# Optimization experiments

Measured on AMD Instinct MI355X. Metric: run time of the kernel, lower is better.

The kernel has to match this reference:

```python
import jax, jax.numpy as jnp
import numpy as np

B, S, D = 4, 2048, 1024
H, HD = 16, 64
MLP = 4 * D
EPS = 1e-6


def _rms_norm(x, scale):
    var = jnp.mean(jnp.square(x), axis=-1, keepdims=True)
    return x * jax.lax.rsqrt(var + EPS) * scale


def setup_inputs() -> dict:
    key = jax.random.key(0)
    ks = jax.random.split(key, 8)
    sd = D ** -0.5
    return {
        "x": jax.random.normal(ks[0], (B, S, D), jnp.float32),
        "pre_norm_scale": jnp.ones((D,), jnp.float32),
        "w_mlp_in": jax.random.normal(ks[1], (D, MLP), jnp.float32) * sd,   # MLPBlockInput, no bias
        "wq": jax.random.normal(ks[2], (D, H, HD), jnp.float32) * sd,
        "wk": jax.random.normal(ks[3], (D, H, HD), jnp.float32) * sd,
        "wv": jax.random.normal(ks[4], (D, H, HD), jnp.float32) * sd,
        "w_mlp_out": jax.random.normal(ks[5], (MLP, D), jnp.float32) * (MLP ** -0.5),
        "b_mlp_out": jnp.zeros((D,), jnp.float32),
        "w_attn_out": jax.random.normal(ks[6], (H, HD, D), jnp.float32) * sd,  # DenseGeneral axis=(-2,-1)
        "b_attn_out": jnp.zeros((D,), jnp.float32),
    }


def reference(x, pre_norm_scale, w_mlp_in, wq, wk, wv, w_mlp_out, b_mlp_out,
              w_attn_out, b_attn_out):
    residual = x
    xn = _rms_norm(x, pre_norm_scale)                      # pre_norm (TPNorm)

    # QKVMLPDense: fused MLP-input + QKV projections
    h = jax.nn.gelu(jnp.einsum("bsd,df->bsf", xn, w_mlp_in))   # [B,S,MLP]
    q = jnp.einsum("bsd,dhk->bshk", xn, wq)                    # [B,S,H,HD]
    k = jnp.einsum("bsd,dhk->bshk", xn, wk)
    v = jnp.einsum("bsd,dhk->bshk", xn, wv)

    # dot_product_attention (mask=None)
    scores = jnp.einsum("bqhd,bkhd->bhqk", q, k) / jnp.sqrt(jnp.asarray(HD, x.dtype))
    probs = jax.nn.softmax(scores, axis=-1)
    attn_v = jnp.einsum("bhqk,bkhd->bqhd", probs, v)           # [B,S,H,HD]

    # AttnMLPOut: mlp_out + attn_out
    mlp_out = jnp.einsum("bsf,fd->bsd", h, w_mlp_out) + b_mlp_out
    attn_out = jnp.einsum("bqhk,hkd->bqd", attn_v, w_attn_out) + b_attn_out
    block_out = mlp_out + attn_out                              # dropout is identity (train=False)
    return residual + block_out
```

## Files before the change

### kernel.cpp

```cpp
#include <hip/hip_runtime.h>
#include <cstdint>
#include <cstddef>

typedef float floatx4 __attribute__((ext_vector_type(4)));
typedef short bf16x8 __attribute__((ext_vector_type(8)));

#define MFMA(a, b, c) __builtin_amdgcn_mfma_f32_16x16x32_bf16((a), (b), (c), 0, 0, 0)

__device__ __forceinline__ unsigned short f2bf(float f) {
  union { float f; unsigned int u; } v; v.f = f;
  unsigned int u = v.u;
  unsigned int r = (u + 0x7FFFu + ((u >> 16) & 1u)) >> 16;
  return (unsigned short)r;
}

__device__ __forceinline__ void gload_lds16(const unsigned short* g, unsigned short* s) {
  __builtin_amdgcn_global_load_lds(
      (const __attribute__((address_space(1))) unsigned int*)g,
      (__attribute__((address_space(3))) unsigned int*)s, 16, 0, 0);
}

__global__ __launch_bounds__(256) void transpose_all(
    const float* __restrict__ w_mlp_in, const float* __restrict__ wq,
    const float* __restrict__ wk, const float* __restrict__ wv,
    const float* __restrict__ w_mlp_out, const float* __restrict__ w_attn_out,
    unsigned short* __restrict__ wcatT, unsigned short* __restrict__ wcat2T) {
  int id = blockIdx.x;
  const float* src; unsigned short* dst; int C, ldd, bx, by, q;
  if (id < 4096)       { src = w_mlp_in;   dst = wcatT;                        C = 4096; ldd = 1024; q = id;         bx = q & 127; by = q >> 7; }
  else if (id < 5120)  { src = wq;         dst = wcatT + (size_t)4096 * 1024;  C = 1024; ldd = 1024; q = id - 4096;  bx = q & 31;  by = q >> 5; }
  else if (id < 6144)  { src = wk;         dst = wcatT + (size_t)5120 * 1024;  C = 1024; ldd = 1024; q = id - 5120;  bx = q & 31;  by = q >> 5; }
  else if (id < 7168)  { src = wv;         dst = wcatT + (size_t)6144 * 1024;  C = 1024; ldd = 1024; q = id - 6144;  bx = q & 31;  by = q >> 5; }
  else if (id < 11264) { src = w_mlp_out;  dst = wcat2T;                       C = 1024; ldd = 5120; q = id - 7168;  bx = q & 31;  by = q >> 5; }
  else                 { src = w_attn_out; dst = wcat2T + 4096;                C = 1024; ldd = 5120; q = id - 11264; bx = q & 31;  by = q >> 5; }
  __shared__ float tile[32][33];
  int tx = threadIdx.x & 31, ty = threadIdx.x >> 5;
#pragma unroll
  for (int i = 0; i < 4; i++) {
    int r = ty + i * 8;
    tile[r][tx] = src[(size_t)(by * 32 + r) * C + bx * 32 + tx];
  }
  __syncthreads();
#pragma unroll
  for (int i = 0; i < 4; i++) {
    int r = ty + i * 8;
    dst[(size_t)(bx * 32 + r) * ldd + by * 32 + tx] = f2bf(tile[tx][r]);
  }
}

__global__ __launch_bounds__(256) void rmsnorm_kernel(
    const float* __restrict__ x, const float* __restrict__ scale,
    unsigned short* __restrict__ xn) {
  int row = blockIdx.x;
  const float4 v = ((const float4*)(x + (size_t)row * 1024))[threadIdx.x];
  float ss = v.x * v.x + v.y * v.y + v.z * v.z + v.w * v.w;
#pragma unroll
  for (int off = 1; off < 64; off <<= 1) ss += __shfl_xor(ss, off, 64);
  __shared__ float ws4[4];
  if ((threadIdx.x & 63) == 0) ws4[threadIdx.x >> 6] = ss;
  __syncthreads();
  float tot = ws4[0] + ws4[1] + ws4[2] + ws4[3];
  float rs = rsqrtf(tot * (1.0f / 1024.0f) + 1e-6f);
  const float4 sc = ((const float4*)scale)[threadIdx.x];
  uint2 o;
  o.x = (unsigned)f2bf(v.x * rs * sc.x) | ((unsigned)f2bf(v.y * rs * sc.y) << 16);
  o.y = (unsigned)f2bf(v.z * rs * sc.z) | ((unsigned)f2bf(v.w * rs * sc.w) << 16);
  ((uint2*)(xn + (size_t)row * 1024))[threadIdx.x] = o;
}

template <int MODE>
__global__ __launch_bounds__(256, 2) void gemm_bt(
    const unsigned short* __restrict__ A, const unsigned short* __restrict__ BT,
    int K, void* __restrict__ outp,
    const float* __restrict__ bias1, const float* __restrict__ bias2,
    const float* __restrict__ resid,
    int msplit, int tm, int tn,
    unsigned short* __restrict__ q_out, unsigned short* __restrict__ k_out,
    unsigned short* __restrict__ v_out) {
  __shared__ unsigned short As[2][128 * 32];
  __shared__ unsigned short Bs[2][128 * 32];

  int id = blockIdx.x + gridDim.x * blockIdx.y;
  int xcd = id & 7, j = id >> 3;
  int mh = xcd % msplit, nq = xcd / msplit;
  int by = mh * tm + j / tn;
  int bx = nq * tn + j % tn;
  int m0 = by * 128, n0 = bx * 128;

  int t = threadIdx.x, lane = t & 63, wave = t >> 6;
  int l15 = lane & 15, quad = lane >> 4;
  int wm = (wave & 1) * 64, wn = (wave >> 1) * 64;

  floatx4 acc[4][4] = {};

  int lr = lane >> 2;
  int lg = (lane & 3) ^ ((lane >> 3) & 3);
  int ch0 = wave * 2, ch1 = wave * 2 + 1;
  const unsigned short* gA0 = A + (size_t)(m0 + ch0 * 16 + lr) * K + lg * 8;
  const unsigned short* gA1 = A + (size_t)(m0 + ch1 * 16 + lr) * K + lg * 8;
  const unsigned short* gB0 = BT + (size_t)(n0 + ch0 * 16 + lr) * K + lg * 8;
  const unsigned short* gB1 = BT + (size_t)(n0 + ch1 * 16 + lr) * K + lg * 8;
  unsigned short* sA0[2] = {&As[0][ch0 * 512 + lane * 8], &As[1][ch0 * 512 + lane * 8]};
  unsigned short* sA1[2] = {&As[0][ch1 * 512 + lane * 8], &As[1][ch1 * 512 + lane * 8]};
  unsigned short* sB0[2] = {&Bs[0][ch0 * 512 + lane * 8], &Bs[1][ch0 * 512 + lane * 8]};
  unsigned short* sB1[2] = {&Bs[0][ch1 * 512 + lane * 8], &Bs[1][ch1 * 512 + lane * 8]};

  int fo = (4 * l15 + (quad ^ ((l15 >> 1) & 3))) * 8;
  int ca = (wm >> 4);
  int cb = (wn >> 4);

  for (int kt = 0; kt < K; kt += 64) {
    __syncthreads();
#pragma unroll
    for (int kk = 0; kk < 2; kk++) {
      int kg = kt + kk * 32;
      gload_lds16(gA0 + kg, sA0[kk]);
      gload_lds16(gA1 + kg, sA1[kk]);
      gload_lds16(gB0 + kg, sB0[kk]);
      gload_lds16(gB1 + kg, sB1[kk]);
    }
    __syncthreads();
#pragma unroll
    for (int kk = 0; kk < 2; kk++) {
      bf16x8 a[4], b[4];
#pragma unroll
      for (int im = 0; im < 4; im++)
        a[im] = *(const bf16x8*)&As[kk][(ca + im) * 512 + fo];
#pragma unroll
      for (int in_ = 0; in_ < 4; in_++)
        b[in_] = *(const bf16x8*)&Bs[kk][(cb + in_) * 512 + fo];
#pragma unroll
      for (int im = 0; im < 4; im++)
#pragma unroll
        for (int in_ = 0; in_ < 4; in_++)
          acc[im][in_] = MFMA(a[im], b[in_], acc[im][in_]);
    }
  }

#pragma unroll
  for (int im = 0; im < 4; im++) {
#pragma unroll
    for (int in_ = 0; in_ < 4; in_++) {
#pragma unroll
      for (int r = 0; r < 4; r++) {
        int row = m0 + wm + im * 16 + quad * 4 + r;
        int col = n0 + wn + in_ * 16 + l15;
        float v = acc[im][in_][r];
        if constexpr (MODE == 6) {
          if (n0 < 4096) {
            float z = 0.7978845608028654f * (v + 0.044715f * v * v * v);
            float e = __expf(2.0f * z);
            float th = 1.0f - 2.0f / (e + 1.0f);
            ((unsigned short*)outp)[(size_t)row * 5120 + col] = f2bf(0.5f * v * (1.0f + th));
          } else {
            int seg = (n0 - 4096) >> 10;
            int cs = col - 4096 - (seg << 10);
            int b_ = row >> 11, s = row & 2047, h = cs >> 6, hd = cs & 63;
            if (seg == 0)
              q_out[(((size_t)(b_ * 16 + h)) * 2048 + s) * 64 + hd] = f2bf(v * 0.125f);
            else if (seg == 1)
              k_out[(((size_t)(b_ * 16 + h)) * 2048 + s) * 64 + hd] = f2bf(v);
            else
              v_out[(((size_t)(b_ * 16 + h)) * 64 + hd) * 2048 + s] = f2bf(v);
          }
        } else {
          size_t idx = (size_t)row * 1024 + col;
          ((float*)outp)[idx] = v + bias1[col] + bias2[col] + resid[idx];
        }
      }
    }
  }
}

__global__ __launch_bounds__(256, 2) void flash_attn(
    const unsigned short* __restrict__ q_buf, const unsigned short* __restrict__ k_buf,
    const unsigned short* __restrict__ v_buf, unsigned short* __restrict__ cat) {
  constexpr int S = 2048, HD = 64;
  constexpr int LK = 72, LV = 72, LP = 68;
  __shared__ unsigned short Ks[64 * LK];
  __shared__ unsigned short Vs[64 * LV];
  __shared__ unsigned short Ps[4][32 * LP];

  int id = blockIdx.x + gridDim.x * blockIdx.y;
  int xcd = id & 7, j = id >> 3;
  int bh = xcd * 8 + (j >> 4);
  int qbk = j & 15;

  int t = threadIdx.x, lane = t & 63, wave = t >> 6;
  int l15 = lane & 15, quad = lane >> 4;

  const unsigned short* qp = q_buf + (size_t)bh * S * HD;
  const unsigned short* kp = k_buf + (size_t)bh * S * HD;
  const unsigned short* vp = v_buf + (size_t)bh * HD * S;

  int q0 = qbk * 128 + wave * 32;
  bf16x8 aQ[2][2];
#pragma unroll
  for (int qf = 0; qf < 2; qf++) {
    aQ[qf][0] = *(const bf16x8*)&qp[(size_t)(q0 + qf * 16 + l15) * HD + quad * 8];
    aQ[qf][1] = *(const bf16x8*)&qp[(size_t)(q0 + qf * 16 + l15) * HD + 32 + quad * 8];
  }

  floatx4 acc_o[2][4] = {};
  float lrow[2][4] = {};

  int kr = t >> 3, kc = (t & 7) * 8;

  uint4 rK0 = *(const uint4*)&kp[(size_t)kr * HD + kc];
  uint4 rK1 = *(const uint4*)&kp[(size_t)(kr + 32) * HD + kc];
  uint4 rV0 = *(const uint4*)&vp[(size_t)kr * S + kc];
  uint4 rV1 = *(const uint4*)&vp[(size_t)(kr + 32) * S + kc];

  for (int kv = 0; kv < S; kv += 64) {
    __syncthreads();
    *(uint4*)&Ks[kr * LK + kc] = rK0;
    *(uint4*)&Ks[(kr + 32) * LK + kc] = rK1;
    *(uint4*)&Vs[kr * LV + kc] = rV0;
    *(uint4*)&Vs[(kr + 32) * LV + kc] = rV1;
    __syncthreads();
    if (kv + 64 < S) {
      rK0 = *(const uint4*)&kp[(size_t)(kv + 64 + kr) * HD + kc];
      rK1 = *(const uint4*)&kp[(size_t)(kv + 64 + kr + 32) * HD + kc];
      rV0 = *(const uint4*)&vp[(size_t)kr * S + kv + 64 + kc];
      rV1 = *(const uint4*)&vp[(size_t)(kr + 32) * S + kv + 64 + kc];
    }

    floatx4 z[2][4];
#pragma unroll
    for (int cg = 0; cg < 4; cg++) {
      bf16x8 bk0 = *(const bf16x8*)&Ks[(cg * 16 + l15) * LK + quad * 8];
      bf16x8 bk1 = *(const bf16x8*)&Ks[(cg * 16 + l15) * LK + 32 + quad * 8];
#pragma unroll
      for (int qf = 0; qf < 2; qf++) {
        floatx4 acc = {};
        acc = MFMA(aQ[qf][0], bk0, acc);
        acc = MFMA(aQ[qf][1], bk1, acc);
        z[qf][cg] = acc;
      }
    }
#pragma unroll
    for (int qf = 0; qf < 2; qf++)
#pragma unroll
      for (int cg = 0; cg < 4; cg++)
#pragma unroll
        for (int r = 0; r < 4; r++) {
          float e = __expf(z[qf][cg][r]);
          lrow[qf][r] += e;
          Ps[wave][(qf * 16 + quad * 4 + r) * LP + cg * 16 + l15] = f2bf(e);
        }
    asm volatile("s_waitcnt lgkmcnt(0)" ::: "memory");
#pragma unroll
    for (int c = 0; c < 2; c++) {
      bf16x8 aP[2];
#pragma unroll
      for (int qf = 0; qf < 2; qf++) {
        const unsigned short* pp = &Ps[wave][(qf * 16 + l15) * LP + c * 32 + quad * 8];
        ((uint2*)&aP[qf])[0] = *(const uint2*)pp;
        ((uint2*)&aP[qf])[1] = *(const uint2*)(pp + 4);
      }
#pragma unroll
      for (int n = 0; n < 4; n++) {
        bf16x8 bv = *(const bf16x8*)&Vs[(n * 16 + l15) * LV + c * 32 + quad * 8];
        acc_o[0][n] = MFMA(aP[0], bv, acc_o[0][n]);
        acc_o[1][n] = MFMA(aP[1], bv, acc_o[1][n]);
      }
    }
  }

#pragma unroll
  for (int qf = 0; qf < 2; qf++)
#pragma unroll
    for (int r = 0; r < 4; r++) {
      float s = lrow[qf][r];
#pragma unroll
      for (int off = 1; off < 16; off <<= 1) s += __shfl_xor(s, off, 16);
      lrow[qf][r] = s;
    }

  int b_ = bh >> 4, h = bh & 15;
#pragma unroll
  for (int qf = 0; qf < 2; qf++)
#pragma unroll
    for (int r = 0; r < 4; r++) {
      float inv = 1.0f / lrow[qf][r];
      int srow = q0 + qf * 16 + quad * 4 + r;
      size_t base = ((size_t)(b_ * 2048 + srow)) * 5120 + 4096 + h * 64;
#pragma unroll
      for (int n = 0; n < 4; n++)
        cat[base + n * 16 + l15] = f2bf(acc_o[qf][n][r] * inv);
    }
}

extern "C" void kernel_launch(void* const* d_in, const int* in_sizes, int n_in,
                              void* d_out, int out_size, void* d_ws, size_t ws_size,
                              hipStream_t stream) {
  (void)in_sizes; (void)n_in; (void)out_size; (void)ws_size;
  const float* x          = (const float*)d_in[0];
  const float* pns        = (const float*)d_in[1];
  const float* w_mlp_in   = (const float*)d_in[2];
  const float* wq         = (const float*)d_in[3];
  const float* wk         = (const float*)d_in[4];
  const float* wv         = (const float*)d_in[5];
  const float* w_mlp_out  = (const float*)d_in[6];
  const float* b_mlp_out  = (const float*)d_in[7];
  const float* w_attn_out = (const float*)d_in[8];
  const float* b_attn_out = (const float*)d_in[9];
  float* out = (float*)d_out;

  char* ws = (char*)d_ws;
  size_t off = 0;
  auto alloc = [&](size_t bytes) {
    void* p = ws + off;
    off += (bytes + 255) & ~(size_t)255;
    return p;
  };
  const size_t M = 8192;
  unsigned short* xn     = (unsigned short*)alloc(M * 1024 * 2);
  unsigned short* wcatT  = (unsigned short*)alloc((size_t)7168 * 1024 * 2);
  unsigned short* wcat2T = (unsigned short*)alloc((size_t)1024 * 5120 * 2);
  unsigned short* cat    = (unsigned short*)alloc(M * 5120 * 2);
  unsigned short* qb     = (unsigned short*)alloc(M * 1024 * 2);
  unsigned short* kb     = (unsigned short*)alloc(M * 1024 * 2);
  unsigned short* vb     = (unsigned short*)alloc(M * 1024 * 2);

  transpose_all<<<dim3(12288), 256, 0, stream>>>(
      w_mlp_in, wq, wk, wv, w_mlp_out, w_attn_out, wcatT, wcat2T);

  rmsnorm_kernel<<<dim3(8192), 256, 0, stream>>>(x, pns, xn);

  gemm_bt<6><<<dim3(56, 64), 256, 0, stream>>>(
      xn, wcatT, 1024, cat, nullptr, nullptr, nullptr, 2, 32, 14, qb, kb, vb);

  flash_attn<<<dim3(16, 64), 256, 0, stream>>>(qb, kb, vb, cat);

  gemm_bt<7><<<dim3(8, 64), 256, 0, stream>>>(
      cat, wcat2T, 5120, out, b_mlp_out, b_attn_out, x, 2, 32, 2, nullptr, nullptr, nullptr);
}
```

Before: 537.9 us.

## Use 256x256 tile GEMM with 8 waves and interleaved async LDS prefetch

Both dense GEMMs move from 128x128 tiles with 4 waves to 256x256 tiles with 8 waves. The main loop is split into four MFMA phases, and global-to-LDS loads for the next k-steps are issued between phases, guarded by explicit barriers, waitcnt and s_setprio. The goal is more operand reuse per LDS byte and better overlap of memory with compute. The trade-off is far fewer blocks: the second GEMM gets only 128 blocks across 256 CUs, which risks poor occupancy and tail effects.

Result: slower. 601.1 us (+11.8%).

```diff
diff --git a/kernel.cpp b/kernel.cpp
--- a/kernel.cpp
+++ b/kernel.cpp
@@ -6,6 +6,8 @@
 typedef short bf16x8 __attribute__((ext_vector_type(8)));
 
 #define MFMA(a, b, c) __builtin_amdgcn_mfma_f32_16x16x32_bf16((a), (b), (c), 0, 0, 0)
+#define BARRIER() __builtin_amdgcn_s_barrier()
+#define LGKM0() asm volatile("s_waitcnt lgkmcnt(0)" ::: "memory")
 
 __device__ __forceinline__ unsigned short f2bf(float f) {
   union { float f; unsigned int u; } v; v.f = f;
@@ -69,7 +71,7 @@
 }
 
 template <int MODE>
-__global__ __launch_bounds__(256, 2) void gemm_bt(
+__global__ __launch_bounds__(512, 2) void gemm256_bt(
     const unsigned short* __restrict__ A, const unsigned short* __restrict__ BT,
     int K, void* __restrict__ outp,
     const float* __restrict__ bias1, const float* __restrict__ bias2,
@@ -77,74 +79,136 @@
     int msplit, int tm, int tn,
     unsigned short* __restrict__ q_out, unsigned short* __restrict__ k_out,
     unsigned short* __restrict__ v_out) {
-  __shared__ unsigned short As[2][128 * 32];
-  __shared__ unsigned short Bs[2][128 * 32];
+  __shared__ unsigned short As[2][2][16][512];
+  __shared__ unsigned short Bs[2][2][16][512];
 
   int id = blockIdx.x + gridDim.x * blockIdx.y;
   int xcd = id & 7, j = id >> 3;
   int mh = xcd % msplit, nq = xcd / msplit;
   int by = mh * tm + j / tn;
   int bx = nq * tn + j % tn;
-  int m0 = by * 128, n0 = bx * 128;
-
-  int t = threadIdx.x, lane = t & 63, wave = t >> 6;
+  int m0 = by * 256, n0 = bx * 256;
+
+  int tid = threadIdx.x, lane = tid & 63, wave = tid >> 6;
   int l15 = lane & 15, quad = lane >> 4;
-  int wm = (wave & 1) * 64, wn = (wave >> 1) * 64;
-
-  floatx4 acc[4][4] = {};
+  int wm = wave >> 2, wn = wave & 3;
 
   int lr = lane >> 2;
   int lg = (lane & 3) ^ ((lane >> 3) & 3);
-  int ch0 = wave * 2, ch1 = wave * 2 + 1;
-  const unsigned short* gA0 = A + (size_t)(m0 + ch0 * 16 + lr) * K + lg * 8;
-  const unsigned short* gA1 = A + (size_t)(m0 + ch1 * 16 + lr) * K + lg * 8;
-  const unsigned short* gB0 = BT + (size_t)(n0 + ch0 * 16 + lr) * K + lg * 8;
-  const unsigned short* gB1 = BT + (size_t)(n0 + ch1 * 16 + lr) * K + lg * 8;
-  unsigned short* sA0[2] = {&As[0][ch0 * 512 + lane * 8], &As[1][ch0 * 512 + lane * 8]};
-  unsigned short* sA1[2] = {&As[0][ch1 * 512 + lane * 8], &As[1][ch1 * 512 + lane * 8]};
-  unsigned short* sB0[2] = {&Bs[0][ch0 * 512 + lane * 8], &Bs[1][ch0 * 512 + lane * 8]};
-  unsigned short* sB1[2] = {&Bs[0][ch1 * 512 + lane * 8], &Bs[1][ch1 * 512 + lane * 8]};
+  const unsigned short* gA = A + (size_t)(m0 + wave * 16 + lr) * K + lg * 8;
+  const unsigned short* gB = BT + (size_t)(n0 + wave * 16 + lr) * K + lg * 8;
+  const size_t rowoff = (size_t)128 * K;
+  int NT = K >> 6;
+
+#define STAGE_A(buf, half, kelem) do {                                        \
+    const unsigned short* _s = gA + (size_t)(half) * rowoff + (kelem);        \
+    gload_lds16(_s,      &As[buf][0][(half) * 8 + wave][lane * 8]);           \
+    gload_lds16(_s + 32, &As[buf][1][(half) * 8 + wave][lane * 8]);           \
+  } while (0)
+#define STAGE_B(buf, half, kelem) do {                                        \
+    const unsigned short* _s = gB + (size_t)(half) * rowoff + (kelem);        \
+    gload_lds16(_s,      &Bs[buf][0][(half) * 8 + wave][lane * 8]);           \
+    gload_lds16(_s + 32, &Bs[buf][1][(half) * 8 + wave][lane * 8]);           \
+  } while (0)
 
   int fo = (4 * l15 + (quad ^ ((l15 >> 1) & 3))) * 8;
-  int ca = (wm >> 4);
-  int cb = (wn >> 4);
-
-  for (int kt = 0; kt < K; kt += 64) {
-    __syncthreads();
-#pragma unroll
-    for (int kk = 0; kk < 2; kk++) {
-      int kg = kt + kk * 32;
-      gload_lds16(gA0 + kg, sA0[kk]);
-      gload_lds16(gA1 + kg, sA1[kk]);
-      gload_lds16(gB0 + kg, sB0[kk]);
-      gload_lds16(gB1 + kg, sB1[kk]);
-    }
-    __syncthreads();
-#pragma unroll
-    for (int kk = 0; kk < 2; kk++) {
-      bf16x8 a[4], b[4];
-#pragma unroll
-      for (int im = 0; im < 4; im++)
-        a[im] = *(const bf16x8*)&As[kk][(ca + im) * 512 + fo];
-#pragma unroll
-      for (int in_ = 0; in_ < 4; in_++)
-        b[in_] = *(const bf16x8*)&Bs[kk][(cb + in_) * 512 + fo];
-#pragma unroll
-      for (int im = 0; im < 4; im++)
-#pragma unroll
-        for (int in_ = 0; in_ < 4; in_++)
-          acc[im][in_] = MFMA(a[im], b[in_], acc[im][in_]);
-    }
-  }
-
-#pragma unroll
-  for (int im = 0; im < 4; im++) {
+
+  floatx4 acc[8][4] = {};
+
+  STAGE_A(0, 0, 0); STAGE_A(0, 1, 0);
+  STAGE_B(0, 0, 0); STAGE_B(0, 1, 0);
+  STAGE_A(1, 0, 64); STAGE_A(1, 1, 64);
+  asm volatile("s_waitcnt vmcnt(4)" ::: "memory");
+  BARRIER();
+
+  for (int t = 0; t < NT; ++t) {
+    int cur = t & 1;
+    bf16x8 a0[4][2], a1[4][2], b[4][2];
+
+#pragma unroll
+    for (int n = 0; n < 2; n++) {
+      b[n][0] = *(const bf16x8*)&Bs[cur][0][wn * 4 + n][fo];
+      b[n][1] = *(const bf16x8*)&Bs[cur][1][wn * 4 + n][fo];
+    }
+#pragma unroll
+    for (int m = 0; m < 4; m++) {
+      a0[m][0] = *(const bf16x8*)&As[cur][0][wm * 8 + m][fo];
+      a0[m][1] = *(const bf16x8*)&As[cur][1][wm * 8 + m][fo];
+    }
+    if (t + 1 < NT) STAGE_B(cur ^ 1, 0, (t + 1) << 6);
+    BARRIER(); LGKM0();
+    __builtin_amdgcn_s_setprio(1);
+#pragma unroll
+    for (int m = 0; m < 4; m++)
+#pragma unroll
+      for (int n = 0; n < 2; n++) {
+        acc[m][n] = MFMA(a0[m][0], b[n][0], acc[m][n]);
+        acc[m][n] = MFMA(a0[m][1], b[n][1], acc[m][n]);
+      }
+    __builtin_amdgcn_s_setprio(0);
+    BARRIER();
+
+#pragma unroll
+    for (int n = 2; n < 4; n++) {
+      b[n][0] = *(const bf16x8*)&Bs[cur][0][wn * 4 + n][fo];
+      b[n][1] = *(const bf16x8*)&Bs[cur][1][wn * 4 + n][fo];
+    }
+    if (t + 1 < NT) STAGE_B(cur ^ 1, 1, (t + 1) << 6);
+    BARRIER(); LGKM0();
+    __builtin_amdgcn_s_setprio(1);
+#pragma unroll
+    for (int m = 0; m < 4; m++)
+#pragma unroll
+      for (int n = 2; n < 4; n++) {
+        acc[m][n] = MFMA(a0[m][0], b[n][0], acc[m][n]);
+        acc[m][n] = MFMA(a0[m][1], b[n][1], acc[m][n]);
+      }
+    __builtin_amdgcn_s_setprio(0);
+    BARRIER();
+
+#pragma unroll
+    for (int m = 0; m < 4; m++) {
+      a1[m][0] = *(const bf16x8*)&As[cur][0][wm * 8 + 4 + m][fo];
+      a1[m][1] = *(const bf16x8*)&As[cur][1][wm * 8 + 4 + m][fo];
+    }
+    BARRIER(); LGKM0();
+    __builtin_amdgcn_s_setprio(1);
+#pragma unroll
+    for (int m = 0; m < 4; m++)
+#pragma unroll
+      for (int n = 0; n < 2; n++) {
+        acc[m + 4][n] = MFMA(a1[m][0], b[n][0], acc[m + 4][n]);
+        acc[m + 4][n] = MFMA(a1[m][1], b[n][1], acc[m + 4][n]);
+      }
+    __builtin_amdgcn_s_setprio(0);
+    BARRIER();
+
+    if (t + 2 < NT) { STAGE_A(cur, 0, (t + 2) << 6); STAGE_A(cur, 1, (t + 2) << 6); }
+    BARRIER();
+    __builtin_amdgcn_s_setprio(1);
+#pragma unroll
+    for (int m = 0; m < 4; m++)
+#pragma unroll
+      for (int n = 2; n < 4; n++) {
+        acc[m + 4][n] = MFMA(a1[m][0], b[n][0], acc[m + 4][n]);
+        acc[m + 4][n] = MFMA(a1[m][1], b[n][1], acc[m + 4][n]);
+      }
+    __builtin_amdgcn_s_setprio(0);
+    if (t + 2 < NT) { asm volatile("s_waitcnt vmcnt(4)" ::: "memory"); }
+    else            { asm volatile("s_waitcnt vmcnt(0)" ::: "memory"); }
+    BARRIER();
+  }
+#undef STAGE_A
+#undef STAGE_B
+
+#pragma unroll
+  for (int im = 0; im < 8; im++) {
 #pragma unroll
     for (int in_ = 0; in_ < 4; in_++) {
 #pragma unroll
       for (int r = 0; r < 4; r++) {
-        int row = m0 + wm + im * 16 + quad * 4 + r;
-        int col = n0 + wn + in_ * 16 + l15;
+        int row = m0 + wm * 128 + im * 16 + quad * 4 + r;
+        int col = n0 + wn * 64 + in_ * 16 + l15;
         float v = acc[im][in_][r];
         if constexpr (MODE == 6) {
           if (n0 < 4096) {
@@ -328,11 +392,11 @@
 
   rmsnorm_kernel<<<dim3(8192), 256, 0, stream>>>(x, pns, xn);
 
-  gemm_bt<6><<<dim3(56, 64), 256, 0, stream>>>(
-      xn, wcatT, 1024, cat, nullptr, nullptr, nullptr, 2, 32, 14, qb, kb, vb);
+  gemm256_bt<6><<<dim3(896), 512, 0, stream>>>(
+      xn, wcatT, 1024, cat, nullptr, nullptr, nullptr, 2, 16, 7, qb, kb, vb);
 
   flash_attn<<<dim3(16, 64), 256, 0, stream>>>(qb, kb, vb, cat);
 
-  gemm_bt<7><<<dim3(8, 64), 256, 0, stream>>>(
-      cat, wcat2T, 5120, out, b_mlp_out, b_attn_out, x, 2, 32, 2, nullptr, nullptr, nullptr);
-}
+  gemm256_bt<7><<<dim3(128), 512, 0, stream>>>(
+      cat, wcat2T, 5120, out, b_mlp_out, b_attn_out, x, 2, 16, 1, nullptr, nullptr, nullptr);
+}
```

## Rewrite GEMMs as 512-thread 256-wide tiles with software-pipelined LDS prefetch

Applied to the files above, without the earlier changes.

Replaces the 128x128 4-wave GEMM with a 512-thread kernel using 256-wide N tiles (256 or 128 rows in M). It adds a ping-pong LDS pipeline that prefetches the next K-tile with global_load_lds while MFMA clusters run, using s_waitcnt vmcnt and setprio instead of full syncthreads. The aim is more reuse per tile and load latency hidden behind compute. The cost is higher LDS and register use per block. Fewer blocks for the output GEMM (256) could also leave CUs underused.

Result: slower. 562.1 us (+4.5%).

```diff
diff --git a/kernel.cpp b/kernel.cpp
--- a/kernel.cpp
+++ b/kernel.cpp
@@ -6,6 +6,7 @@
 typedef short bf16x8 __attribute__((ext_vector_type(8)));
 
 #define MFMA(a, b, c) __builtin_amdgcn_mfma_f32_16x16x32_bf16((a), (b), (c), 0, 0, 0)
+#define BARRIER() __builtin_amdgcn_s_barrier()
 
 __device__ __forceinline__ unsigned short f2bf(float f) {
   union { float f; unsigned int u; } v; v.f = f;
@@ -68,8 +69,8 @@
   ((uint2*)(xn + (size_t)row * 1024))[threadIdx.x] = o;
 }
 
-template <int MODE>
-__global__ __launch_bounds__(256, 2) void gemm_bt(
+template <int MODE, int MR>
+__global__ __launch_bounds__(512, 2) void gemm256_bt(
     const unsigned short* __restrict__ A, const unsigned short* __restrict__ BT,
     int K, void* __restrict__ outp,
     const float* __restrict__ bias1, const float* __restrict__ bias2,
@@ -77,74 +78,118 @@
     int msplit, int tm, int tn,
     unsigned short* __restrict__ q_out, unsigned short* __restrict__ k_out,
     unsigned short* __restrict__ v_out) {
-  __shared__ unsigned short As[2][128 * 32];
-  __shared__ unsigned short Bs[2][128 * 32];
+  constexpr int RCA = MR * 2;
+  constexpr int NSA = MR / 4;
+  __shared__ unsigned short As[2][2][RCA][512];
+  __shared__ unsigned short Bs[2][2][16][512];
 
   int id = blockIdx.x + gridDim.x * blockIdx.y;
   int xcd = id & 7, j = id >> 3;
   int mh = xcd % msplit, nq = xcd / msplit;
   int by = mh * tm + j / tn;
   int bx = nq * tn + j % tn;
-  int m0 = by * 128, n0 = bx * 128;
-
-  int t = threadIdx.x, lane = t & 63, wave = t >> 6;
+  int m0 = by * (MR * 32), n0 = bx * 256;
+
+  int tid = threadIdx.x, lane = tid & 63, wave = tid >> 6;
   int l15 = lane & 15, quad = lane >> 4;
-  int wm = (wave & 1) * 64, wn = (wave >> 1) * 64;
-
-  floatx4 acc[4][4] = {};
+  int wm = wave >> 2, wn = wave & 3;
 
   int lr = lane >> 2;
   int lg = (lane & 3) ^ ((lane >> 3) & 3);
-  int ch0 = wave * 2, ch1 = wave * 2 + 1;
-  const unsigned short* gA0 = A + (size_t)(m0 + ch0 * 16 + lr) * K + lg * 8;
-  const unsigned short* gA1 = A + (size_t)(m0 + ch1 * 16 + lr) * K + lg * 8;
-  const unsigned short* gB0 = BT + (size_t)(n0 + ch0 * 16 + lr) * K + lg * 8;
-  const unsigned short* gB1 = BT + (size_t)(n0 + ch1 * 16 + lr) * K + lg * 8;
-  unsigned short* sA0[2] = {&As[0][ch0 * 512 + lane * 8], &As[1][ch0 * 512 + lane * 8]};
-  unsigned short* sA1[2] = {&As[0][ch1 * 512 + lane * 8], &As[1][ch1 * 512 + lane * 8]};
-  unsigned short* sB0[2] = {&Bs[0][ch0 * 512 + lane * 8], &Bs[1][ch0 * 512 + lane * 8]};
-  unsigned short* sB1[2] = {&Bs[0][ch1 * 512 + lane * 8], &Bs[1][ch1 * 512 + lane * 8]};
+  const unsigned short* gA = A + (size_t)(m0 + wave * 16 + lr) * K + lg * 8;
+  const unsigned short* gB = BT + (size_t)(n0 + wave * 16 + lr) * K + lg * 8;
+  int NT = K >> 6;
+
+#define STAGE_A(buf, kk, kel) do {                                        \
+    _Pragma("unroll")                                                     \
+    for (int s = 0; s < NSA; s++)                                         \
+      gload_lds16(gA + (size_t)s * 128 * K + (kel) + (kk) * 32,           \
+                  &As[buf][kk][wave + s * 8][lane * 8]);                  \
+  } while (0)
+#define STAGE_B(buf, kk, kel) do {                                        \
+    _Pragma("unroll")                                                     \
+    for (int s = 0; s < 2; s++)                                           \
+      gload_lds16(gB + (size_t)s * 128 * K + (kel) + (kk) * 32,           \
+                  &Bs[buf][kk][wave + s * 8][lane * 8]);                  \
+  } while (0)
+#define WAITV() do {                                                      \
+    if constexpr (NSA == 2) asm volatile("s_waitcnt vmcnt(4)" ::: "memory"); \
+    else                    asm volatile("s_waitcnt vmcnt(3)" ::: "memory"); \
+  } while (0)
+#define RD_A(dst, buf, kk, half) do {                                     \
+    _Pragma("unroll")                                                     \
+    for (int mf = 0; mf < MR / 2; mf++)                                   \
+      dst[mf] = *(const bf16x8*)&As[buf][kk][wm * MR + (half) * (MR / 2) + mf][fo]; \
+  } while (0)
+#define RD_B(dst, buf, kk) do {                                           \
+    _Pragma("unroll")                                                     \
+    for (int n = 0; n < 4; n++)                                           \
+      dst[n] = *(const bf16x8*)&Bs[buf][kk][wn * 4 + n][fo];              \
+  } while (0)
+#define CLUSTER(abase, af, bf) do {                                       \
+    __builtin_amdgcn_s_setprio(1);                                        \
+    _Pragma("unroll")                                                     \
+    for (int mf = 0; mf < MR / 2; mf++)                                   \
+      _Pragma("unroll")                                                   \
+      for (int n = 0; n < 4; n++)                                         \
+        acc[(abase) + mf][n] = MFMA(af[mf], bf[n], acc[(abase) + mf][n]); \
+    __builtin_amdgcn_s_setprio(0);                                        \
+  } while (0)
 
   int fo = (4 * l15 + (quad ^ ((l15 >> 1) & 3))) * 8;
-  int ca = (wm >> 4);
-  int cb = (wn >> 4);
-
-  for (int kt = 0; kt < K; kt += 64) {
-    __syncthreads();
-#pragma unroll
-    for (int kk = 0; kk < 2; kk++) {
-      int kg = kt + kk * 32;
-      gload_lds16(gA0 + kg, sA0[kk]);
-      gload_lds16(gA1 + kg, sA1[kk]);
-      gload_lds16(gB0 + kg, sB0[kk]);
-      gload_lds16(gB1 + kg, sB1[kk]);
-    }
-    __syncthreads();
-#pragma unroll
-    for (int kk = 0; kk < 2; kk++) {
-      bf16x8 a[4], b[4];
-#pragma unroll
-      for (int im = 0; im < 4; im++)
-        a[im] = *(const bf16x8*)&As[kk][(ca + im) * 512 + fo];
-#pragma unroll
-      for (int in_ = 0; in_ < 4; in_++)
-        b[in_] = *(const bf16x8*)&Bs[kk][(cb + in_) * 512 + fo];
-#pragma unroll
-      for (int im = 0; im < 4; im++)
-#pragma unroll
-        for (int in_ = 0; in_ < 4; in_++)
-          acc[im][in_] = MFMA(a[im], b[in_], acc[im][in_]);
-    }
-  }
-
-#pragma unroll
-  for (int im = 0; im < 4; im++) {
+
+  floatx4 acc[MR][4] = {};
+  bf16x8 aL0[MR / 2], aH0[MR / 2], aL1[MR / 2], aH1[MR / 2], bk0[4], bk1[4];
+
+  STAGE_A(0, 0, 0); STAGE_B(0, 0, 0); STAGE_A(0, 1, 0); STAGE_B(0, 1, 0);
+  WAITV();
+  BARRIER();
+  __builtin_amdgcn_sched_barrier(0);
+  RD_A(aL0, 0, 0, 0); RD_B(bk0, 0, 0);
+
+  for (int t = 0; t < NT; ++t) {
+    int cur = t & 1, nxt = cur ^ 1, k1 = (t + 1) << 6;
+    bool pf = (t + 1 < NT);
+    if (pf) STAGE_A(nxt, 0, k1);
+    RD_A(aH0, cur, 0, 1);
+    CLUSTER(0, aL0, bk0);
+    if (pf) {
+      STAGE_B(nxt, 0, k1);
+      WAITV();
+    } else {
+      asm volatile("s_waitcnt vmcnt(0)" ::: "memory");
+    }
+    BARRIER();
+    __builtin_amdgcn_sched_barrier(0);
+    RD_A(aL1, cur, 1, 0); RD_B(bk1, cur, 1);
+    CLUSTER(MR / 2, aH0, bk0);
+    if (pf) STAGE_A(nxt, 1, k1);
+    RD_A(aH1, cur, 1, 1);
+    CLUSTER(0, aL1, bk1);
+    if (pf) {
+      STAGE_B(nxt, 1, k1);
+      WAITV();
+      BARRIER();
+      __builtin_amdgcn_sched_barrier(0);
+      RD_A(aL0, nxt, 0, 0); RD_B(bk0, nxt, 0);
+    }
+    CLUSTER(MR / 2, aH1, bk1);
+  }
+#undef STAGE_A
+#undef STAGE_B
+#undef WAITV
+#undef RD_A
+#undef RD_B
+#undef CLUSTER
+
+#pragma unroll
+  for (int im = 0; im < MR; im++) {
 #pragma unroll
     for (int in_ = 0; in_ < 4; in_++) {
 #pragma unroll
       for (int r = 0; r < 4; r++) {
-        int row = m0 + wm + im * 16 + quad * 4 + r;
-        int col = n0 + wn + in_ * 16 + l15;
+        int row = m0 + wm * (MR * 16) + im * 16 + quad * 4 + r;
+        int col = n0 + wn * 64 + in_ * 16 + l15;
         float v = acc[im][in_][r];
         if constexpr (MODE == 6) {
           if (n0 < 4096) {
@@ -328,11 +373,11 @@
 
   rmsnorm_kernel<<<dim3(8192), 256, 0, stream>>>(x, pns, xn);
 
-  gemm_bt<6><<<dim3(56, 64), 256, 0, stream>>>(
-      xn, wcatT, 1024, cat, nullptr, nullptr, nullptr, 2, 32, 14, qb, kb, vb);
+  gemm256_bt<6, 8><<<dim3(896), 512, 0, stream>>>(
+      xn, wcatT, 1024, cat, nullptr, nullptr, nullptr, 2, 16, 7, qb, kb, vb);
 
   flash_attn<<<dim3(16, 64), 256, 0, stream>>>(qb, kb, vb, cat);
 
-  gemm_bt<7><<<dim3(8, 64), 256, 0, stream>>>(
-      cat, wcat2T, 5120, out, b_mlp_out, b_attn_out, x, 2, 32, 2, nullptr, nullptr, nullptr);
-}
+  gemm256_bt<7, 4><<<dim3(256), 512, 0, stream>>>(
+      cat, wcat2T, 5120, out, b_mlp_out, b_attn_out, x, 8, 8, 4, nullptr, nullptr, nullptr);
+}
```

## Double-buffer K/V tiles in flash attention and merge rmsnorm into prep kernel

Applied to the files above, without the earlier changes.

Flash attention now keeps two LDS buffers for K and V. The next tile is written to the spare buffer while the current one is consumed, and the global prefetch for two tiles ahead is issued after the QK MFMAs. This cuts the per-iteration barriers from two to one and hides more load latency. Separately, the weight transpose and rmsnorm kernels are merged into a single launch, saving one kernel launch. The extra LDS may lower occupancy.

Result: slower. 549.7 us (+2.2%).

```diff
diff --git a/kernel.cpp b/kernel.cpp
--- a/kernel.cpp
+++ b/kernel.cpp
@@ -20,12 +20,33 @@
       (__attribute__((address_space(3))) unsigned int*)s, 16, 0, 0);
 }
 
-__global__ __launch_bounds__(256) void transpose_all(
+__global__ __launch_bounds__(256) void prep_all(
     const float* __restrict__ w_mlp_in, const float* __restrict__ wq,
     const float* __restrict__ wk, const float* __restrict__ wv,
     const float* __restrict__ w_mlp_out, const float* __restrict__ w_attn_out,
-    unsigned short* __restrict__ wcatT, unsigned short* __restrict__ wcat2T) {
+    const float* __restrict__ x, const float* __restrict__ pns,
+    unsigned short* __restrict__ wcatT, unsigned short* __restrict__ wcat2T,
+    unsigned short* __restrict__ xn) {
+  __shared__ float tile[32][33];
+  __shared__ float ws4[4];
   int id = blockIdx.x;
+  if (id >= 12288) {
+    int row = id - 12288;
+    const float4 v = ((const float4*)(x + (size_t)row * 1024))[threadIdx.x];
+    float ss = v.x * v.x + v.y * v.y + v.z * v.z + v.w * v.w;
+#pragma unroll
+    for (int off = 1; off < 64; off <<= 1) ss += __shfl_xor(ss, off, 64);
+    if ((threadIdx.x & 63) == 0) ws4[threadIdx.x >> 6] = ss;
+    __syncthreads();
+    float tot = ws4[0] + ws4[1] + ws4[2] + ws4[3];
+    float rs = rsqrtf(tot * (1.0f / 1024.0f) + 1e-6f);
+    const float4 sc = ((const float4*)pns)[threadIdx.x];
+    uint2 o;
+    o.x = (unsigned)f2bf(v.x * rs * sc.x) | ((unsigned)f2bf(v.y * rs * sc.y) << 16);
+    o.y = (unsigned)f2bf(v.z * rs * sc.z) | ((unsigned)f2bf(v.w * rs * sc.w) << 16);
+    ((uint2*)(xn + (size_t)row * 1024))[threadIdx.x] = o;
+    return;
+  }
   const float* src; unsigned short* dst; int C, ldd, bx, by, q;
   if (id < 4096)       { src = w_mlp_in;   dst = wcatT;                        C = 4096; ldd = 1024; q = id;         bx = q & 127; by = q >> 7; }
   else if (id < 5120)  { src = wq;         dst = wcatT + (size_t)4096 * 1024;  C = 1024; ldd = 1024; q = id - 4096;  bx = q & 31;  by = q >> 5; }
@@ -33,7 +54,6 @@
   else if (id < 7168)  { src = wv;         dst = wcatT + (size_t)6144 * 1024;  C = 1024; ldd = 1024; q = id - 6144;  bx = q & 31;  by = q >> 5; }
   else if (id < 11264) { src = w_mlp_out;  dst = wcat2T;                       C = 1024; ldd = 5120; q = id - 7168;  bx = q & 31;  by = q >> 5; }
   else                 { src = w_attn_out; dst = wcat2T + 4096;                C = 1024; ldd = 5120; q = id - 11264; bx = q & 31;  by = q >> 5; }
-  __shared__ float tile[32][33];
   int tx = threadIdx.x & 31, ty = threadIdx.x >> 5;
 #pragma unroll
   for (int i = 0; i < 4; i++) {
@@ -46,26 +66,6 @@
     int r = ty + i * 8;
     dst[(size_t)(bx * 32 + r) * ldd + by * 32 + tx] = f2bf(tile[tx][r]);
   }
-}
-
-__global__ __launch_bounds__(256) void rmsnorm_kernel(
-    const float* __restrict__ x, const float* __restrict__ scale,
-    unsigned short* __restrict__ xn) {
-  int row = blockIdx.x;
-  const float4 v = ((const float4*)(x + (size_t)row * 1024))[threadIdx.x];
-  float ss = v.x * v.x + v.y * v.y + v.z * v.z + v.w * v.w;
-#pragma unroll
-  for (int off = 1; off < 64; off <<= 1) ss += __shfl_xor(ss, off, 64);
-  __shared__ float ws4[4];
-  if ((threadIdx.x & 63) == 0) ws4[threadIdx.x >> 6] = ss;
-  __syncthreads();
-  float tot = ws4[0] + ws4[1] + ws4[2] + ws4[3];
-  float rs = rsqrtf(tot * (1.0f / 1024.0f) + 1e-6f);
-  const float4 sc = ((const float4*)scale)[threadIdx.x];
-  uint2 o;
-  o.x = (unsigned)f2bf(v.x * rs * sc.x) | ((unsigned)f2bf(v.y * rs * sc.y) << 16);
-  o.y = (unsigned)f2bf(v.z * rs * sc.z) | ((unsigned)f2bf(v.w * rs * sc.w) << 16);
-  ((uint2*)(xn + (size_t)row * 1024))[threadIdx.x] = o;
 }
 
 template <int MODE>
@@ -177,8 +177,8 @@
     const unsigned short* __restrict__ v_buf, unsigned short* __restrict__ cat) {
   constexpr int S = 2048, HD = 64;
   constexpr int LK = 72, LV = 72, LP = 68;
-  __shared__ unsigned short Ks[64 * LK];
-  __shared__ unsigned short Vs[64 * LV];
+  __shared__ unsigned short Ks[2][64 * LK];
+  __shared__ unsigned short Vs[2][64 * LV];
   __shared__ unsigned short Ps[4][32 * LP];
 
   int id = blockIdx.x + gridDim.x * blockIdx.y;
@@ -210,26 +210,31 @@
   uint4 rK1 = *(const uint4*)&kp[(size_t)(kr + 32) * HD + kc];
   uint4 rV0 = *(const uint4*)&vp[(size_t)kr * S + kc];
   uint4 rV1 = *(const uint4*)&vp[(size_t)(kr + 32) * S + kc];
+  *(uint4*)&Ks[0][kr * LK + kc] = rK0;
+  *(uint4*)&Ks[0][(kr + 32) * LK + kc] = rK1;
+  *(uint4*)&Vs[0][kr * LV + kc] = rV0;
+  *(uint4*)&Vs[0][(kr + 32) * LV + kc] = rV1;
+  rK0 = *(const uint4*)&kp[(size_t)(64 + kr) * HD + kc];
+  rK1 = *(const uint4*)&kp[(size_t)(64 + kr + 32) * HD + kc];
+  rV0 = *(const uint4*)&vp[(size_t)kr * S + 64 + kc];
+  rV1 = *(const uint4*)&vp[(size_t)(kr + 32) * S + 64 + kc];
+  asm volatile("s_waitcnt lgkmcnt(0)" ::: "memory");
+  __syncthreads();
 
   for (int kv = 0; kv < S; kv += 64) {
-    __syncthreads();
-    *(uint4*)&Ks[kr * LK + kc] = rK0;
-    *(uint4*)&Ks[(kr + 32) * LK + kc] = rK1;
-    *(uint4*)&Vs[kr * LV + kc] = rV0;
-    *(uint4*)&Vs[(kr + 32) * LV + kc] = rV1;
-    __syncthreads();
+    int cur = (kv >> 6) & 1;
     if (kv + 64 < S) {
-      rK0 = *(const uint4*)&kp[(size_t)(kv + 64 + kr) * HD + kc];
-      rK1 = *(const uint4*)&kp[(size_t)(kv + 64 + kr + 32) * HD + kc];
-      rV0 = *(const uint4*)&vp[(size_t)kr * S + kv + 64 + kc];
-      rV1 = *(const uint4*)&vp[(size_t)(kr + 32) * S + kv + 64 + kc];
+      *(uint4*)&Ks[cur ^ 1][kr * LK + kc] = rK0;
+      *(uint4*)&Ks[cur ^ 1][(kr + 32) * LK + kc] = rK1;
+      *(uint4*)&Vs[cur ^ 1][kr * LV + kc] = rV0;
+      *(uint4*)&Vs[cur ^ 1][(kr + 32) * LV + kc] = rV1;
     }
 
     floatx4 z[2][4];
 #pragma unroll
     for (int cg = 0; cg < 4; cg++) {
-      bf16x8 bk0 = *(const bf16x8*)&Ks[(cg * 16 + l15) * LK + quad * 8];
-      bf16x8 bk1 = *(const bf16x8*)&Ks[(cg * 16 + l15) * LK + 32 + quad * 8];
+      bf16x8 bk0 = *(const bf16x8*)&Ks[cur][(cg * 16 + l15) * LK + quad * 8];
+      bf16x8 bk1 = *(const bf16x8*)&Ks[cur][(cg * 16 + l15) * LK + 32 + quad * 8];
 #pragma unroll
       for (int qf = 0; qf < 2; qf++) {
         floatx4 acc = {};
@@ -238,6 +243,12 @@
         z[qf][cg] = acc;
       }
     }
+    if (kv + 128 < S) {
+      rK0 = *(const uint4*)&kp[(size_t)(kv + 128 + kr) * HD + kc];
+      rK1 = *(const uint4*)&kp[(size_t)(kv + 128 + kr + 32) * HD + kc];
+      rV0 = *(const uint4*)&vp[(size_t)kr * S + kv + 128 + kc];
+      rV1 = *(const uint4*)&vp[(size_t)(kr + 32) * S + kv + 128 + kc];
+    }
 #pragma unroll
     for (int qf = 0; qf < 2; qf++)
 #pragma unroll
@@ -260,11 +271,12 @@
       }
 #pragma unroll
       for (int n = 0; n < 4; n++) {
-        bf16x8 bv = *(const bf16x8*)&Vs[(n * 16 + l15) * LV + c * 32 + quad * 8];
+        bf16x8 bv = *(const bf16x8*)&Vs[cur][(n * 16 + l15) * LV + c * 32 + quad * 8];
         acc_o[0][n] = MFMA(aP[0], bv, acc_o[0][n]);
         acc_o[1][n] = MFMA(aP[1], bv, acc_o[1][n]);
       }
     }
+    __syncthreads();
   }
 
 #pragma unroll
@@ -323,10 +335,8 @@
   unsigned short* kb     = (unsigned short*)alloc(M * 1024 * 2);
   unsigned short* vb     = (unsigned short*)alloc(M * 1024 * 2);
 
-  transpose_all<<<dim3(12288), 256, 0, stream>>>(
-      w_mlp_in, wq, wk, wv, w_mlp_out, w_attn_out, wcatT, wcat2T);
-
-  rmsnorm_kernel<<<dim3(8192), 256, 0, stream>>>(x, pns, xn);
+  prep_all<<<dim3(20480), 256, 0, stream>>>(
+      w_mlp_in, wq, wk, wv, w_mlp_out, w_attn_out, x, pns, wcatT, wcat2T, xn);
 
   gemm_bt<6><<<dim3(56, 64), 256, 0, stream>>>(
       xn, wcatT, 1024, cat, nullptr, nullptr, nullptr, 2, 32, 14, qb, kb, vb);
```
